# Optimization experiments

Measured on AMD Instinct MI355X. Metric: run time of the kernel, lower is better.

Reference implementation:

```python
import jax, jax.numpy as jnp
import numpy as np
from jax import lax

HID = 512
NEG = -1e30

def conv2d(x, w, pad):
    # x: [N,C,H,W], w: [O,I,kh,kw]
    return lax.conv_general_dilated(x, w, (1, 1), [(pad, pad), (pad, pad)],
                                    dimension_numbers=('NCHW', 'OIHW', 'NCHW'))

def maxpool3s2p1(x):
    return lax.reduce_window(x, -jnp.inf, lax.max, (1, 1, 3, 3), (1, 1, 2, 2),
                             [(0, 0), (0, 0), (1, 1), (1, 1)])

def setup_inputs() -> dict:
    key = jax.random.key(0)
    ks = jax.random.split(key, 12)
    N, B = 128, 16
    gid = jnp.repeat(jnp.arange(B), N // B).astype(jnp.float32)  # sorted group ids
    rois = jnp.concatenate([gid[:, None], jax.random.uniform(ks[0], (N, 4))], axis=1)
    interact_feat = jax.random.normal(ks[1], (N, 2304, 1, 16, 16), jnp.float32)
    bbox_feat = jax.random.normal(ks[2], (N, 1024, 4, 7, 7), jnp.float32)
    s = lambda k, sh: jax.random.normal(k, sh, jnp.float32) * 0.02
    return {
        'rois': rois,
        'interact_feat': interact_feat,
        'bbox_feat': bbox_feat,
        'w_reduce': s(ks[3], (HID, 2304, 1, 1)),
        'w_rsize': s(ks[4], (HID, HID, 3, 3)),
        'wq': s(ks[5], (HID, HID, 3, 3)),
        'wk': s(ks[6], (HID, HID, 3, 3)),
        'wv': s(ks[7], (HID, HID, 3, 3)),
        'w1': s(ks[8], (HID, HID, 3, 3)),
        'gamma': jnp.ones((HID,), jnp.float32),
        'beta': jnp.zeros((HID,), jnp.float32),
        'w_fc': s(ks[9], (HID, 2 * HID)),
    }

def reference(rois, interact_feat, bbox_feat, w_reduce, w_rsize, wq, wk, wv, w1, gamma, beta, w_fc):
    f = interact_feat[:, :, 0]                      # squeeze(2): [N,2304,16,16]
    f = jax.nn.relu(conv2d(f, w_reduce, 0))         # [N,512,16,16]
    f = conv2d(f, w_rsize, 0)                       # no padding -> [N,512,14,14]
    f = maxpool3s2p1(f)                             # [N,512,7,7]

    gid = rois[:, 0].astype(jnp.int32)
    mask = gid[:, None] == gid[None, :]             # [N,N] same-group mask (vectorizes ragged loop)

    q = conv2d(f, wq, 1)
    k = conv2d(f, wk, 1)
    v = conv2d(f, wv, 1)
    # per-pixel attention across rois within each group
    att = jnp.einsum('ichw,jchw->ijhw', q, k) / jnp.sqrt(jnp.asarray(HID, f.dtype))
    att = jnp.where(mask[:, :, None, None], att, NEG)
    att = jax.nn.softmax(att, axis=1)               # softmax over key rois (dim=1)
    virt = jnp.einsum('ijhw,jchw->ichw', att, v)    # [N,512,7,7]

    # GroupNorm(1, C): normalize over (C,H,W), per-channel affine
    mu = virt.mean(axis=(1, 2, 3), keepdims=True)
    var = virt.var(axis=(1, 2, 3), keepdims=True)
    virt = (virt - mu) / jnp.sqrt(var + 1e-5)
    virt = virt * gamma[None, :, None, None] + beta[None, :, None, None]
    virt = jax.nn.relu(virt)
    virt = conv2d(virt, w1, 1)                      # dropout = identity in eval

    ho = (f + virt).mean(axis=(2, 3))               # gap1 -> [N,512]
    ob = bbox_feat.mean(axis=(2, 3, 4))             # gap2 -> [N,1024]
    ob = jax.nn.relu(ob @ w_fc.T)                   # fc1 -> [N,512]
    return jnp.concatenate([ho, ob], axis=1)        # [N,1024]
```

## Files before the change

### kernel.cpp

```cpp
#include <hip/hip_runtime.h>
#include <hip/hip_bf16.h>
#include <math.h>

typedef __bf16 bf16;
typedef __bf16 v8bf __attribute__((ext_vector_type(8)));
typedef float f32x4 __attribute__((ext_vector_type(4)));

#define GLDS16(g, l) __builtin_amdgcn_global_load_lds( \
    (const __attribute__((address_space(1))) void*)(g), \
    (__attribute__((address_space(3))) void*)(l), 16, 0, 0)

__device__ __forceinline__ int xcd_swz(int bid, int nwg) {
  int xcd = bid & 7, off = bid >> 3;
  int q = nwg >> 3, r = nwg & 7;
  return (xcd < r ? xcd * (q + 1) : r * (q + 1) + (xcd - r) * q) + off;
}

#define SBZ __builtin_amdgcn_sched_barrier(0)
#define BARR __builtin_amdgcn_s_barrier()

#define RD_B8(SLOTB) do { \
  _Pragma("unroll") for (int _j = 0; _j < 4; ++_j) \
  _Pragma("unroll") for (int _kk = 0; _kk < 2; ++_kk) { \
    int _r = (wn & 1) * 64 + _j * 16 + l15; \
    int _c = (_kk * 64 + kq) ^ ((_r & 7) << 4); \
    bfr[_j][_kk] = *(const v8bf*)((SLOTB) + _r * 128 + _c); } } while (0)

#define RD_A4(SLOTA, CL) do { \
  _Pragma("unroll") for (int _f = 0; _f < 2; ++_f) \
  _Pragma("unroll") for (int _kk = 0; _kk < 2; ++_kk) { \
    int _r = (CL) * 32 + _f * 16 + l15; \
    int _c = (_kk * 64 + kq) ^ ((_r & 7) << 4); \
    af[_f][_kk] = *(const v8bf*)((SLOTA) + _r * 128 + _c); } } while (0)

#define MMA16(CL) do { \
  __builtin_amdgcn_s_setprio(1); \
  _Pragma("unroll") for (int _f = 0; _f < 2; ++_f) \
  _Pragma("unroll") for (int _j = 0; _j < 4; ++_j) \
  _Pragma("unroll") for (int _kk = 0; _kk < 2; ++_kk) \
    acc[(CL)*2 + _f][_j] = __builtin_amdgcn_mfma_f32_16x16x32_bf16( \
        af[_f][_kk], bfr[_j][_kk], acc[(CL)*2 + _f][_j], 0, 0, 0); \
  __builtin_amdgcn_s_setprio(0); } while (0)

#define VM4 asm volatile("s_waitcnt vmcnt(4)" ::: "memory")
#define VM0 asm volatile("s_waitcnt vmcnt(0)" ::: "memory")

#define PH8_ITER(STGA, STGB, NIT)                                        \
  {                                                                      \
    int t1k = 2 * iv + 1, t2k = 2 * iv + 2, t3k = 2 * iv + 3;            \
    bool s2 = (iv + 1 < (NIT));                                          \
    RD_B8(bslot0); RD_A4(aslot0, 0); STGA(0, t1k, 1);                    \
    SBZ; BARR; SBZ; MMA16(0); SBZ; BARR;                                 \
    RD_A4(aslot0, 1); STGA(1, t1k, 1);                                   \
    SBZ; BARR; SBZ; MMA16(1); SBZ; BARR;                                 \
    RD_A4(aslot0, 2); if (s2) STGB(0, t2k, 0);                           \
    SBZ; BARR; SBZ; MMA16(2); SBZ; BARR;                                 \
    RD_A4(aslot0, 3); if (s2) STGB(1, t2k, 0);                           \
    SBZ; BARR; SBZ; MMA16(3); SBZ;                                       \
    if (s2) { VM4; } else { VM0; }                                       \
    BARR;                                                                \
    RD_B8(bslot1); RD_A4(aslot1, 0); if (s2) STGA(0, t2k, 0);            \
    SBZ; BARR; SBZ; MMA16(0); SBZ; BARR;                                 \
    RD_A4(aslot1, 1); if (s2) STGA(1, t2k, 0);                           \
    SBZ; BARR; SBZ; MMA16(1); SBZ; BARR;                                 \
    RD_A4(aslot1, 2); if (s2) STGB(0, t3k, 1);                           \
    SBZ; BARR; SBZ; MMA16(2); SBZ; BARR;                                 \
    RD_A4(aslot1, 3); if (s2) STGB(1, t3k, 1);                           \
    SBZ; BARR; SBZ; MMA16(3); SBZ;                                       \
    if (s2) { VM4; } else { VM0; }                                       \
    BARR;                                                                \
  }

__global__ __launch_bounds__(512, 2)
void k_gemm_reduce(const bf16* __restrict__ A, const bf16* __restrict__ B,
                   bf16* __restrict__ f1, int mbase)
{
  extern __shared__ char lds[];
  const int s = xcd_swz(blockIdx.x, gridDim.x);
  const int by = s & 1, bx = s >> 1;
  const int t = threadIdx.x, lane = t & 63, w = t >> 6;
  const int wm = w >> 2, wn = w & 3;
  const int l15 = lane & 15, kq = (lane >> 4) << 4;
  const int tr64 = t >> 3;
  const int lb = ((t & 7) << 4) ^ ((tr64 & 7) << 4);
  const int t16 = t * 16;
  const char* aslot0 = lds + wm * 16384;
  const char* aslot1 = lds + 65536 + wm * 16384;
  const char* bslot0 = lds + 32768 + (wn >> 1) * 16384;
  const char* bslot1 = lds + 98304 + (wn >> 1) * 16384;
  const char* paA[2][2]; const char* paB[2][2];
  #pragma unroll
  for (int h = 0; h < 2; ++h)
    #pragma unroll
    for (int c = 0; c < 2; ++c) {
      paA[h][c] = (const char*)A + (size_t)(bx * 256 + h * 128 + c * 64 + tr64) * 4608 + lb;
      paB[h][c] = (const char*)B + (size_t)(by * 256 + h * 128 + c * 64 + tr64) * 4608 + lb;
    }
  #define GR_STGA(h, kt, d) do { \
    GLDS16(paA[h][0] + (size_t)(kt) * 128, lds + (d) * 65536 + (h) * 16384 + t16); \
    GLDS16(paA[h][1] + (size_t)(kt) * 128, lds + (d) * 65536 + (h) * 16384 + 8192 + t16); } while (0)
  #define GR_STGB(h, kt, d) do { \
    GLDS16(paB[h][0] + (size_t)(kt) * 128, lds + (d) * 65536 + 32768 + (h) * 16384 + t16); \
    GLDS16(paB[h][1] + (size_t)(kt) * 128, lds + (d) * 65536 + 32768 + (h) * 16384 + 8192 + t16); } while (0)

  f32x4 acc[8][4] = {};
  v8bf bfr[4][2], af[2][2];
  GR_STGB(0, 0, 0); GR_STGB(1, 0, 0); GR_STGA(0, 0, 0); GR_STGA(1, 0, 0);
  GR_STGB(0, 1, 1); GR_STGB(1, 1, 1);
  VM4; BARR;
  for (int iv = 0; iv < 18; ++iv) PH8_ITER(GR_STGA, GR_STGB, 18);
  const int rbase = (lane >> 4) << 2, cl = lane & 15;
  #pragma unroll
  for (int i = 0; i < 8; ++i)
    #pragma unroll
    for (int j = 0; j < 4; ++j)
      #pragma unroll
      for (int r = 0; r < 4; ++r) {
        int row = mbase + bx * 256 + wm * 128 + i * 16 + rbase + r;
        int col = by * 256 + wn * 64 + j * 16 + cl;
        f1[(size_t)row * 512 + col] = (bf16)fmaxf(acc[i][j][r], 0.f);
      }
}

__global__ __launch_bounds__(512, 2)
void k_conv_rsize(const bf16* __restrict__ f1, const bf16* __restrict__ wt,
                  bf16* __restrict__ f14)
{
  extern __shared__ char lds[];
  const int s = xcd_swz(blockIdx.x, gridDim.x);
  const int by = s & 1, bx = s >> 1;
  const int t = threadIdx.x, lane = t & 63, w = t >> 6;
  const int wm = w >> 2, wn = w & 3;
  const int l15 = lane & 15, kq = (lane >> 4) << 4;
  const int tr64 = t >> 3;
  const int lb = ((t & 7) << 4) ^ ((tr64 & 7) << 4);
  const int t16 = t * 16;
  const char* aslot0 = lds + wm * 16384;
  const char* aslot1 = lds + 65536 + wm * 16384;
  const char* bslot0 = lds + 32768 + (wn >> 1) * 16384;
  const char* bslot1 = lds + 98304 + (wn >> 1) * 16384;
  int ab[2][2]; const char* pwB[2][2];
  #pragma unroll
  for (int h = 0; h < 2; ++h)
    #pragma unroll
    for (int c = 0; c < 2; ++c) {
      int m = bx * 256 + h * 128 + c * 64 + tr64;
      int n = m / 196, rem = m - n * 196;
      int y = rem / 14, x = rem - 14 * (rem / 14);
      ab[h][c] = n * 256 + y * 16 + x;
      pwB[h][c] = (const char*)wt + (size_t)(by * 256 + h * 128 + c * 64 + tr64) * 1024 + lb;
    }
  const char* f1c = (const char*)f1 + lb;
  #define CR_STGA(h, kt, d) do { \
    int _tap = (kt) >> 3, _ko = ((kt) & 7) << 7; \
    int _dy = (_tap * 11) >> 5, _dx = _tap - _dy * 3; \
    int _df = (_dy * 16 + _dx) << 10; \
    GLDS16(f1c + ((size_t)ab[h][0] << 10) + _df + _ko, lds + (d) * 65536 + (h) * 16384 + t16); \
    GLDS16(f1c + ((size_t)ab[h][1] << 10) + _df + _ko, lds + (d) * 65536 + (h) * 16384 + 8192 + t16); } while (0)
  #define CR_STGB(h, kt, d) do { \
    int _tap = (kt) >> 3, _ko = ((kt) & 7) << 7; \
    GLDS16(pwB[h][0] + (size_t)_tap * 524288 + _ko, lds + (d) * 65536 + 32768 + (h) * 16384 + t16); \
    GLDS16(pwB[h][1] + (size_t)_tap * 524288 + _ko, lds + (d) * 65536 + 32768 + (h) * 16384 + 8192 + t16); } while (0)

  f32x4 acc[8][4] = {};
  v8bf bfr[4][2], af[2][2];
  CR_STGB(0, 0, 0); CR_STGB(1, 0, 0); CR_STGA(0, 0, 0); CR_STGA(1, 0, 0);
  CR_STGB(0, 1, 1); CR_STGB(1, 1, 1);
  VM4; BARR;
  for (int iv = 0; iv < 36; ++iv) PH8_ITER(CR_STGA, CR_STGB, 36);
  const int rbase = (lane >> 4) << 2, cl = lane & 15;
  #pragma unroll
  for (int i = 0; i < 8; ++i)
    #pragma unroll
    for (int j = 0; j < 4; ++j)
      #pragma unroll
      for (int r = 0; r < 4; ++r) {
        int row = bx * 256 + wm * 128 + i * 16 + rbase + r;
        int col = by * 256 + wn * 64 + j * 16 + cl;
        f14[(size_t)row * 512 + col] = (bf16)acc[i][j][r];
      }
}

__global__ __launch_bounds__(512, 2)
void k_conv_qkv(const bf16* __restrict__ fin, const bf16* __restrict__ wt,
                bf16* __restrict__ qkv, const bf16* __restrict__ zp,
                const float* __restrict__ bbox, float* __restrict__ obm)
{
  extern __shared__ char lds[];
  const int t = threadIdx.x;
  if (blockIdx.x >= 150) {
    int bid = blockIdx.x - 150;
    int n = bid >> 3;
    int c = (bid & 7) * 128 + (t >> 2);
    int seg = t & 3;
    const float4* p4 = (const float4*)(bbox + ((size_t)n * 1024 + c) * 196);
    float sum = 0.f;
    for (int k = seg; k < 49; k += 4) { float4 ww = p4[k]; sum += ww.x + ww.y + ww.z + ww.w; }
    sum += __shfl_xor(sum, 1);
    sum += __shfl_xor(sum, 2);
    if (seg == 0) obm[n * 1024 + c] = sum * (1.f / 196.f);
    return;
  }
  const int s = xcd_swz(blockIdx.x, 150);
  const int q6 = s % 6, bx = s / 6;
  const int tensor = q6 >> 1, byh = q6 & 1;
  const char* wtc = (const char*)wt + (size_t)tensor * 4718592;
  bf16* outp = qkv + (size_t)tensor * 3211264;
  const int lane = t & 63, w = t >> 6;
  const int wm = w >> 2, wn = w & 3;
  const int l15 = lane & 15, kq = (lane >> 4) << 4;
  const int tr64 = t >> 3;
  const int lb = ((t & 7) << 4) ^ ((tr64 & 7) << 4);
  const int t16 = t * 16;
  const char* aslot0 = lds + wm * 16384;
  const char* aslot1 = lds + 65536 + wm * 16384;
  const char* bslot0 = lds + 32768 + (wn >> 1) * 16384;
  const char* bslot1 = lds + 98304 + (wn >> 1) * 16384;
  int nb[2][2], py[2][2], px[2][2]; const char* pwB[2][2];
  #pragma unroll
  for (int h = 0; h < 2; ++h)
    #pragma unroll
    for (int c = 0; c < 2; ++c) {
      int m = bx * 256 + h * 128 + c * 64 + tr64;
      if (m > 6271) m = 6271;
      int n = m / 49, rem = m - n * 49;
      nb[h][c] = n * 49;
      py[h][c] = rem / 7 - 1;
      px[h][c] = rem - 7 * (rem / 7) - 1;
      pwB[h][c] = wtc + (size_t)(byh * 256 + h * 128 + c * 64 + tr64) * 1024 + lb;
    }
  const char* finc = (const char*)fin + lb;
  const char* zpc = (const char*)zp;
  #define QK_STGA(h, kt, d) do { \
    int _tap = (kt) >> 3, _ko = ((kt) & 7) << 7; \
    int _dy = (_tap * 11) >> 5, _dx = _tap - _dy * 3; \
    _Pragma("unroll") for (int _c = 0; _c < 2; ++_c) { \
      int _iy = py[h][_c] + _dy, _ix = px[h][_c] + _dx; \
      const char* _sp = ((unsigned)_iy < 7u && (unsigned)_ix < 7u) \
          ? finc + (size_t)(nb[h][_c] + _iy * 7 + _ix) * 1024 + _ko : zpc; \
      GLDS16(_sp, lds + (d) * 65536 + (h) * 16384 + _c * 8192 + t16); } } while (0)
  #define QK_STGB(h, kt, d) do { \
    int _tap = (kt) >> 3, _ko = ((kt) & 7) << 7; \
    GLDS16(pwB[h][0] + (size_t)_tap * 524288 + _ko, lds + (d) * 65536 + 32768 + (h) * 16384 + t16); \
    GLDS16(pwB[h][1] + (size_t)_tap * 524288 + _ko, lds + (d) * 65536 + 32768 + (h) * 16384 + 8192 + t16); } while (0)

  f32x4 acc[8][4] = {};
  v8bf bfr[4][2], af[2][2];
  QK_STGB(0, 0, 0); QK_STGB(1, 0, 0); QK_STGA(0, 0, 0); QK_STGA(1, 0, 0);
  QK_STGB(0, 1, 1); QK_STGB(1, 1, 1);
  VM4; BARR;
  for (int iv = 0; iv < 36; ++iv) PH8_ITER(QK_STGA, QK_STGB, 36);
  const int rbase = (lane >> 4) << 2, cl = lane & 15;
  #pragma unroll
  for (int i = 0; i < 8; ++i)
    #pragma unroll
    for (int j = 0; j < 4; ++j)
      #pragma unroll
      for (int r = 0; r < 4; ++r) {
        int row = bx * 256 + wm * 128 + i * 16 + rbase + r;
        if (row < 6272) {
          int col = byh * 256 + wn * 64 + j * 16 + cl;
          outp[(size_t)row * 512 + col] = (bf16)acc[i][j][r];
        }
      }
}

__device__ __forceinline__ void tile_compute(const char* ldsA, const char* ldsB,
                                             f32x4 (&acc)[4][4], int wr, int wc, int lane) {
  const int l15 = lane & 15;
  const int colb = (lane >> 4) << 4;
  #pragma unroll
  for (int kk = 0; kk < 2; ++kk) {
    v8bf a[4], b[4];
    #pragma unroll
    for (int i = 0; i < 4; ++i) {
      int ra = wr * 64 + i * 16 + l15;
      int ca = ((kk << 6) | colb) ^ ((ra & 7) << 4);
      a[i] = *(const v8bf*)(ldsA + ra * 128 + ca);
    }
    #pragma unroll
    for (int j = 0; j < 4; ++j) {
      int rb = wc * 64 + j * 16 + l15;
      int cb = ((kk << 6) | colb) ^ ((rb & 7) << 4);
      b[j] = *(const v8bf*)(ldsB + rb * 128 + cb);
    }
    __builtin_amdgcn_s_setprio(1);
    #pragma unroll
    for (int i = 0; i < 4; ++i)
      #pragma unroll
      for (int j = 0; j < 4; ++j)
        acc[i][j] = __builtin_amdgcn_mfma_f32_16x16x32_bf16(a[i], b[j], acc[i][j], 0, 0, 0);
    __builtin_amdgcn_s_setprio(0);
  }
}

#define PIPELINE_LOOP(NK)                                                   \
  stage(0, lds);                                                            \
  stage(1, lds + 32768);                                                    \
  int cur = 0;                                                              \
  for (int ks = 0; ks < (NK) - 1; ++ks) {                                   \
    asm volatile("s_waitcnt vmcnt(8)" ::: "memory");                        \
    __builtin_amdgcn_s_barrier();                                           \
    __builtin_amdgcn_sched_barrier(0);                                      \
    tile_compute(lds + cur * 32768, lds + cur * 32768 + 16384, acc, wr, wc, lane); \
    __builtin_amdgcn_sched_barrier(0);                                      \
    __builtin_amdgcn_s_barrier();                                           \
    __builtin_amdgcn_sched_barrier(0);                                      \
    if (ks + 2 < (NK)) stage(ks + 2, lds + cur * 32768);                    \
    cur ^= 1;                                                               \
  }                                                                         \
  asm volatile("s_waitcnt vmcnt(0)" ::: "memory");                          \
  __builtin_amdgcn_s_barrier();                                             \
  __builtin_amdgcn_sched_barrier(0);                                        \
  tile_compute(lds + cur * 32768, lds + cur * 32768 + 16384, acc, wr, wc, lane);

__global__ __launch_bounds__(256)
void k_gemm_s(const bf16* __restrict__ A_s, const bf16* __restrict__ w1r,
              float* __restrict__ out)
{
  __shared__ __attribute__((aligned(16))) char lds[65536];
  const int by = blockIdx.x, kspl = blockIdx.y;
  const int t = threadIdx.x, lane = t & 63, w = t >> 6, wr = w >> 1, wc = w & 1;
  const int tr = t >> 3;
  const int cphys = ((t & 7) << 4) ^ ((tr & 7) << 4);
  const char* pa[4]; const char* pb[4];
  #pragma unroll
  for (int i = 0; i < 4; ++i) {
    int r = i * 32 + tr;
    pa[i] = (const char*)A_s + (size_t)r * 9216 + kspl * 2304 + cphys;
    pb[i] = (const char*)w1r + (size_t)(by * 128 + r) * 9216 + kspl * 2304 + cphys;
  }
  const int lo = t * 16;
  auto stage = [&](int ks, char* base) {
    #pragma unroll
    for (int i = 0; i < 4; ++i) GLDS16(pa[i] + ks * 128, base + lo + i * 4096);
    #pragma unroll
    for (int i = 0; i < 4; ++i) GLDS16(pb[i] + ks * 128, base + 16384 + lo + i * 4096);
  };
  f32x4 acc[4][4] = {};
  PIPELINE_LOOP(18)
  const int rb = (lane >> 4) << 2, cl = lane & 15;
  #pragma unroll
  for (int i = 0; i < 4; ++i)
    #pragma unroll
    for (int j = 0; j < 4; ++j)
      #pragma unroll
      for (int r = 0; r < 4; ++r) {
        int row = wr * 64 + i * 16 + rb + r;
        int col = by * 128 + wc * 64 + j * 16 + cl;
        atomicAdd(&out[(size_t)row * 1024 + col], acc[i][j][r]);
      }
}

__global__ void k_tin(const float* __restrict__ in, bf16* __restrict__ A1, int n0)
{
  __shared__ float tile[64][36];
  const int k0 = blockIdx.x * 64, p0 = blockIdx.y * 32, nl = blockIdx.z;
  const int n = n0 + nl;
  const int t = threadIdx.x;
  const float* src = in + (size_t)n * 2304 * 256;
  #pragma unroll
  for (int rep = 0; rep < 2; ++rep) {
    int idx = t + rep * 256;
    int row = idx >> 3, c4 = (idx & 7) * 4;
    float4 v = *(const float4*)(src + (size_t)(k0 + row) * 256 + p0 + c4);
    tile[row][c4] = v.x; tile[row][c4 + 1] = v.y;
    tile[row][c4 + 2] = v.z; tile[row][c4 + 3] = v.w;
  }
  __syncthreads();
  const int pl = t >> 3, ke = (t & 7) * 8;
  v8bf o;
  #pragma unroll
  for (int e = 0; e < 8; ++e) o[e] = (bf16)tile[ke + e][pl];
  bf16* dst = A1 + (size_t)nl * 256 * 2304;
  *(v8bf*)(dst + (size_t)(p0 + pl) * 2304 + k0 + ke) = o;
}

__global__ void k_wprep(const float* __restrict__ wred, const float* __restrict__ s0,
                        const float* __restrict__ s1, const float* __restrict__ s2,
                        const float* __restrict__ s3, const float* __restrict__ s4,
                        bf16* __restrict__ wrb, bf16* __restrict__ wt,
                        bf16* __restrict__ w1r)
{
  if (blockIdx.x < 1152) {
    int idx = (blockIdx.x * 256 + threadIdx.x) * 4;
    float4 v = *(const float4*)(wred + idx);
    bf16* d = wrb + idx;
    d[0] = (bf16)v.x; d[1] = (bf16)v.y; d[2] = (bf16)v.z; d[3] = (bf16)v.w;
    return;
  }
  int bid = blockIdx.x - 1152;
  int by = bid >> 10, bx = bid & 1023;
  const float* src;
  switch (by) {
    case 0: src = s0; break; case 1: src = s1; break; case 2: src = s2; break;
    case 3: src = s3; break; default: src = s4; break;
  }
  int q = bx * 256 + threadIdx.x;
  const float* sp = src + (size_t)q * 9;
  float tmp[9];
  #pragma unroll
  for (int e = 0; e < 9; ++e) tmp[e] = sp[e];
  if (by < 4) {
    bf16* dst = wt + (size_t)by * 2359296;
    #pragma unroll
    for (int e = 0; e < 9; ++e) dst[(size_t)e * 262144 + q] = (bf16)tmp[e];
  } else {
    int co = q >> 9, ci = q & 511;
    #pragma unroll
    for (int e = 0; e < 9; ++e) w1r[(size_t)(co * 9 + e) * 512 + ci] = (bf16)tmp[e];
  }
}

__global__ void k_pool(const bf16* __restrict__ f14, bf16* __restrict__ f7b)
{
  int idx = blockIdx.x * 256 + threadIdx.x;
  int c2 = idx & 255;
  int pp = idx >> 8;
  int n = pp / 49, p7 = pp - n * 49;
  int y = p7 / 7, x = p7 - 7 * (p7 / 7);
  int y0 = 2 * y - 1, x0 = 2 * x - 1;
  const unsigned* f14u = (const unsigned*)f14;
  float m0 = -3.4e38f, m1 = -3.4e38f;
  #pragma unroll
  for (int dy = 0; dy < 3; ++dy) {
    int iy = y0 + dy; if ((unsigned)iy >= 14u) continue;
    #pragma unroll
    for (int dx = 0; dx < 3; ++dx) {
      int ix = x0 + dx; if ((unsigned)ix >= 14u) continue;
      unsigned vv = f14u[(size_t)(n * 196 + iy * 14 + ix) * 256 + c2];
      m0 = fmaxf(m0, __builtin_bit_cast(float, vv << 16));
      m1 = fmaxf(m1, __builtin_bit_cast(float, vv & 0xffff0000u));
    }
  }
  bf16 b0 = (bf16)m0, b1 = (bf16)m1;
  unsigned pk = (unsigned)__builtin_bit_cast(unsigned short, b0)
              | ((unsigned)__builtin_bit_cast(unsigned short, b1) << 16);
  ((unsigned*)f7b)[idx] = pk;
}

__global__ __launch_bounds__(256)
void k_attn(const bf16* __restrict__ q, const bf16* __restrict__ k,
            const bf16* __restrict__ v, const float* __restrict__ rois,
            float* __restrict__ virt)
{
  const int p = blockIdx.x, g = blockIdx.y, t = threadIdx.x;
  __shared__ float sS[8][9];
  __shared__ float sP[8][9];
  __shared__ __attribute__((aligned(16))) bf16 sV[8][512];
  {
    int u = t;
    #pragma unroll
    for (int rep = 0; rep < 2; ++rep, u += 256) {
      int j = u >> 6, ch = u & 63;
      *(v8bf*)&sV[j][ch * 8] = *(const v8bf*)(v + ((size_t)(g * 8 + j) * 49 + p) * 512 + ch * 8);
    }
  }
  int pi = t >> 2, ls = t & 3;
  int i = pi >> 3, j = pi & 7;
  const bf16* qi = q + ((size_t)(g * 8 + i) * 49 + p) * 512;
  const bf16* kj = k + ((size_t)(g * 8 + j) * 49 + p) * 512;
  float s = 0.f;
  for (int ch = ls * 16; ch < ls * 16 + 16; ++ch) {
    v8bf a = *(const v8bf*)(qi + ch * 8);
    v8bf b = *(const v8bf*)(kj + ch * 8);
    #pragma unroll
    for (int e = 0; e < 8; ++e) s += (float)a[e] * (float)b[e];
  }
  s += __shfl_xor(s, 1);
  s += __shfl_xor(s, 2);
  if (ls == 0) sS[i][j] = s * 0.04419417382415922f;
  __syncthreads();
  if (t < 8) {
    float gi = rois[(g * 8 + t) * 5];
    float pv[8]; float mx = -3.4e38f;
    #pragma unroll
    for (int jj = 0; jj < 8; ++jj) {
      float gj = rois[(g * 8 + jj) * 5];
      float sv = (gi == gj) ? sS[t][jj] : -1e30f;
      pv[jj] = sv; mx = fmaxf(mx, sv);
    }
    float sum = 0.f;
    #pragma unroll
    for (int jj = 0; jj < 8; ++jj) { float e = expf(pv[jj] - mx); pv[jj] = e; sum += e; }
    float inv = 1.f / sum;
    #pragma unroll
    for (int jj = 0; jj < 8; ++jj) sP[t][jj] = pv[jj] * inv;
  }
  __syncthreads();
  int i2 = t >> 5, c0 = (t & 31) * 16;
  float o[16];
  #pragma unroll
  for (int e = 0; e < 16; ++e) o[e] = 0.f;
  #pragma unroll
  for (int jj = 0; jj < 8; ++jj) {
    float ww = sP[i2][jj];
    v8bf v0 = *(const v8bf*)&sV[jj][c0];
    v8bf v1 = *(const v8bf*)&sV[jj][c0 + 8];
    #pragma unroll
    for (int e = 0; e < 8; ++e) { o[e] += ww * (float)v0[e]; o[8 + e] += ww * (float)v1[e]; }
  }
  float* dst = virt + ((size_t)(g * 8 + i2) * 49 + p) * 512 + c0;
  #pragma unroll
  for (int e = 0; e < 16; ++e) dst[e] = o[e];
}

__global__ __launch_bounds__(512)
void k_ln_fc(const float* __restrict__ virt, const float* __restrict__ gamma,
             const float* __restrict__ beta, const bf16* __restrict__ f7b,
             bf16* __restrict__ A_s,
             const float* __restrict__ obm, const float* __restrict__ wfc,
             float* __restrict__ out)
{
  const int t = threadIdx.x;
  if (blockIdx.x >= 128) {
    __shared__ float sO[1024];
    int n = blockIdx.x - 128;
    for (int u = t; u < 1024; u += 512) sO[u] = obm[n * 1024 + u];
    __syncthreads();
    const float4* wp = (const float4*)(wfc + (size_t)t * 1024);
    float s = 0.f;
    for (int c4 = 0; c4 < 256; ++c4) {
      float4 w = wp[c4];
      s += w.x * sO[c4 * 4] + w.y * sO[c4 * 4 + 1] + w.z * sO[c4 * 4 + 2] + w.w * sO[c4 * 4 + 3];
    }
    out[n * 1024 + 512 + t] = fmaxf(s, 0.f);
    return;
  }
  const int n = blockIdx.x;
  const float* p = virt + (size_t)n * 25088 + t;
  float xv[49];
  float s1 = 0.f, s2 = 0.f;
  #pragma unroll
  for (int pp = 0; pp < 49; ++pp) {
    float x = p[pp * 512];
    xv[pp] = x; s1 += x; s2 += x * x;
  }
  __shared__ float r1[512], r2[512];
  r1[t] = s1; r2[t] = s2; __syncthreads();
  for (int off = 256; off; off >>= 1) {
    if (t < off) { r1[t] += r1[t + off]; r2[t] += r2[t + off]; }
    __syncthreads();
  }
  float mu = r1[0] * (1.f / 25088.f);
  float var = r2[0] * (1.f / 25088.f) - mu * mu;
  float rstd = rsqrtf(var + 1e-5f);
  float g = gamma[t], be = beta[t];
  const bf16* fp = f7b + (size_t)n * 25088 + t;
  float T = 0, R0 = 0, R6 = 0, C0 = 0, C6 = 0;
  float X00 = 0, X06 = 0, X60 = 0, X66 = 0, F = 0;
  #pragma unroll
  for (int pp = 0; pp < 49; ++pp) {
    const int u = pp / 7, v = pp - 7 * (pp / 7);
    float y = fmaxf((xv[pp] - mu) * rstd * g + be, 0.f);
    T += y;
    if (u == 0) R0 += y;
    if (u == 6) R6 += y;
    if (v == 0) C0 += y;
    if (v == 6) C6 += y;
    if (pp == 0)  X00 = y;
    if (pp == 6)  X06 = y;
    if (pp == 42) X60 = y;
    if (pp == 48) X66 = y;
    F += (float)fp[pp * 512];
  }
  float sv[9] = { T-R6-C6+X66, T-R6, T-R6-C0+X60,
                  T-C6,        T,    T-C0,
                  T-R0-C6+X06, T-R0, T-R0-C0+X00 };
  bf16* Ap = A_s + (size_t)n * 4608 + t;
  #pragma unroll
  for (int tap = 0; tap < 9; ++tap)
    Ap[tap * 512] = (bf16)(sv[tap] * (1.f / 49.f));
  out[n * 1024 + t] = F * (1.f / 49.f);
}

extern "C" void kernel_launch(void* const* d_in, const int* in_sizes, int n_in,
                              void* d_out, int out_size, void* d_ws, size_t ws_size,
                              hipStream_t stream) {
  const float* rois     = (const float*)d_in[0];
  const float* interact = (const float*)d_in[1];
  const float* bbox     = (const float*)d_in[2];
  const float* w_reduce = (const float*)d_in[3];
  const float* w_rsize  = (const float*)d_in[4];
  const float* wq       = (const float*)d_in[5];
  const float* wk       = (const float*)d_in[6];
  const float* wv       = (const float*)d_in[7];
  const float* w1       = (const float*)d_in[8];
  const float* gamma    = (const float*)d_in[9];
  const float* beta     = (const float*)d_in[10];
  const float* wfc      = (const float*)d_in[11];
  float* out = (float*)d_out;
  char* ws = (char*)d_ws;

  size_t o = 0;
  auto take = [&](size_t sz) { size_t r = o; o += (sz + 255) & ~(size_t)255; return r; };
  bf16*  wrb   = (bf16*)(ws + take(2359296));
  bf16*  wt    = (bf16*)(ws + take(18874368));
  bf16*  w1r   = (bf16*)(ws + take(4718592));
  char*  Rf1   = ws + take(33554432);
  bf16*  f7b   = (bf16*)(ws + take(6422528));
  float* virt  = (float*)(ws + take(12845056));
  bf16*  A_s   = (bf16*)(ws + take(1179648));
  float* obm   = (float*)(ws + take(524288));
  bf16*  zp    = (bf16*)(ws + take(256));
  size_t fixedEnd = o;
  const size_t A1_FULL = 150994944;
  bool full = (ws_size >= fixedEnd + A1_FULL);
  bf16* A1  = (bf16*)(ws + fixedEnd);
  bf16* f14 = (bf16*)(ws + fixedEnd);

  bf16* f1 = (bf16*)Rf1;
  bf16* qb = (bf16*)Rf1;
  bf16* kb = qb + 3211264;
  bf16* vb = kb + 3211264;

  hipMemsetAsync(zp, 0, 256, stream);

  k_wprep<<<6272, 256, 0, stream>>>(w_reduce, w_rsize, wq, wk, wv, w1, wrb, wt, w1r);

  if (full) {
    k_tin<<<dim3(36, 8, 128), 256, 0, stream>>>(interact, A1, 0);
    k_gemm_reduce<<<256, 512, 131072, stream>>>(A1, wrb, f1, 0);
  } else {
    for (int ch = 0; ch < 4; ++ch) {
      k_tin<<<dim3(36, 8, 32), 256, 0, stream>>>(interact, A1, ch * 32);
      k_gemm_reduce<<<64, 512, 131072, stream>>>(A1, wrb, f1, ch * 8192);
    }
  }

  k_conv_rsize<<<196, 512, 131072, stream>>>(f1, wt, f14);
  k_pool<<<6272, 256, 0, stream>>>(f14, f7b);

  k_conv_qkv<<<1174, 512, 131072, stream>>>(f7b, wt + (size_t)1 * 2359296, qb, zp, bbox, obm);

  k_attn<<<dim3(49, 16), 256, 0, stream>>>(qb, kb, vb, rois, virt);

  k_ln_fc<<<256, 512, 0, stream>>>(virt, gamma, beta, f7b, A_s, obm, wfc, out);

  k_gemm_s<<<dim3(4, 4), 256, 0, stream>>>(A_s, w1r, out);
}
```

Measured before the change: 514.7 us.

## Overlap input transpose of next chunk with reduce GEMM of current chunk

Fuses the weight-prep kernel with the first chunk's input transpose into one launch. The 1x1 reduce GEMM is then split into four chunked launches, and each launch also carries the blocks that transpose the next chunk's input. The aim is to hide the memory-bound transpose behind the compute-bound GEMM and cut kernel launches. The cost is heavy extra blocks that each reserve 128KB of dynamic LDS, so transpose blocks may limit occupancy. The full-workspace path is dropped, so the GEMM always runs as four 64-block launches.

```diff
diff --git a/kernel.cpp b/kernel.cpp
--- a/kernel.cpp
+++ b/kernel.cpp
@@ -71,14 +71,93 @@
     BARR;                                                                \
   }
 
+__device__ __forceinline__ void tin_block(const float* __restrict__ in,
+                                          bf16* __restrict__ A1,
+                                          int n, int kt, int pt, int t, char* ldsbuf)
+{
+  float* tile = (float*)ldsbuf;
+  const int k0 = kt * 64, p0 = pt * 64;
+  const float* src = in + (size_t)n * 589824;
+  #pragma unroll
+  for (int rep = 0; rep < 2; ++rep) {
+    int idx = t + rep * 512;
+    int row = idx >> 4, c4 = (idx & 15) * 4;
+    float4 v = *(const float4*)(src + (size_t)(k0 + row) * 256 + p0 + c4);
+    tile[row * 69 + c4]     = v.x; tile[row * 69 + c4 + 1] = v.y;
+    tile[row * 69 + c4 + 2] = v.z; tile[row * 69 + c4 + 3] = v.w;
+  }
+  __syncthreads();
+  const int pl = t >> 3, ke = (t & 7) * 8;
+  v8bf o;
+  #pragma unroll
+  for (int e = 0; e < 8; ++e) o[e] = (bf16)tile[(ke + e) * 69 + pl];
+  *(v8bf*)(A1 + (size_t)(n * 256 + p0 + pl) * 2304 + k0 + ke) = o;
+}
+
+__global__ __launch_bounds__(512)
+void k_prep(const float* __restrict__ interact, bf16* __restrict__ A1,
+            const float* __restrict__ wred, const float* __restrict__ s0,
+            const float* __restrict__ s1, const float* __restrict__ s2,
+            const float* __restrict__ s3, const float* __restrict__ s4,
+            bf16* __restrict__ wrb, bf16* __restrict__ wt,
+            bf16* __restrict__ w1r)
+{
+  __shared__ __attribute__((aligned(16))) char ldsb[17664];
+  const int t = threadIdx.x;
+  if (blockIdx.x < 4608) {
+    int bid = blockIdx.x;
+    int kt = bid % 36, rest = bid / 36;
+    int pt = rest & 3, nl = rest >> 2;
+    tin_block(interact, A1, nl, kt, pt, t, ldsb);
+    return;
+  }
+  int bid2 = blockIdx.x - 4608;
+  if (bid2 < 576) {
+    int idx = (bid2 * 512 + t) * 4;
+    float4 v = *(const float4*)(wred + idx);
+    bf16* d = wrb + idx;
+    d[0] = (bf16)v.x; d[1] = (bf16)v.y; d[2] = (bf16)v.z; d[3] = (bf16)v.w;
+    return;
+  }
+  int bid3 = bid2 - 576;
+  int by = bid3 >> 9, bx = bid3 & 511;
+  const float* src;
+  switch (by) {
+    case 0: src = s0; break; case 1: src = s1; break; case 2: src = s2; break;
+    case 3: src = s3; break; default: src = s4; break;
+  }
+  int q = bx * 512 + t;
+  const float* sp = src + (size_t)q * 9;
+  float tmp[9];
+  #pragma unroll
+  for (int e = 0; e < 9; ++e) tmp[e] = sp[e];
+  if (by < 4) {
+    bf16* dst = wt + (size_t)by * 2359296;
+    #pragma unroll
+    for (int e = 0; e < 9; ++e) dst[(size_t)e * 262144 + q] = (bf16)tmp[e];
+  } else {
+    int co = q >> 9, ci = q & 511;
+    #pragma unroll
+    for (int e = 0; e < 9; ++e) w1r[(size_t)(co * 9 + e) * 512 + ci] = (bf16)tmp[e];
+  }
+}
+
 __global__ __launch_bounds__(512, 2)
-void k_gemm_reduce(const bf16* __restrict__ A, const bf16* __restrict__ B,
-                   bf16* __restrict__ f1, int mbase)
+void k_tg(const float* __restrict__ interact, bf16* __restrict__ A1,
+          const bf16* __restrict__ B, bf16* __restrict__ f1, int chunk)
 {
   extern __shared__ char lds[];
-  const int s = xcd_swz(blockIdx.x, gridDim.x);
-  const int by = s & 1, bx = s >> 1;
-  const int t = threadIdx.x, lane = t & 63, w = t >> 6;
+  const int t = threadIdx.x;
+  if (blockIdx.x >= 64) {
+    int bid = blockIdx.x - 64;
+    int kt = bid % 36, rest = bid / 36;
+    int pt = rest & 3, nl = rest >> 2;
+    tin_block(interact, A1, (chunk + 1) * 32 + nl, kt, pt, t, lds);
+    return;
+  }
+  const int s = xcd_swz(blockIdx.x, 64);
+  const int by = s & 1, bx = chunk * 32 + (s >> 1);
+  const int lane = t & 63, w = t >> 6;
   const int wm = w >> 2, wn = w & 3;
   const int l15 = lane & 15, kq = (lane >> 4) << 4;
   const int tr64 = t >> 3;
@@ -93,22 +172,22 @@
   for (int h = 0; h < 2; ++h)
     #pragma unroll
     for (int c = 0; c < 2; ++c) {
-      paA[h][c] = (const char*)A + (size_t)(bx * 256 + h * 128 + c * 64 + tr64) * 4608 + lb;
+      paA[h][c] = (const char*)A1 + (size_t)(bx * 256 + h * 128 + c * 64 + tr64) * 4608 + lb;
       paB[h][c] = (const char*)B + (size_t)(by * 256 + h * 128 + c * 64 + tr64) * 4608 + lb;
     }
-  #define GR_STGA(h, kt, d) do { \
+  #define GT_STGA(h, kt, d) do { \
     GLDS16(paA[h][0] + (size_t)(kt) * 128, lds + (d) * 65536 + (h) * 16384 + t16); \
     GLDS16(paA[h][1] + (size_t)(kt) * 128, lds + (d) * 65536 + (h) * 16384 + 8192 + t16); } while (0)
-  #define GR_STGB(h, kt, d) do { \
+  #define GT_STGB(h, kt, d) do { \
     GLDS16(paB[h][0] + (size_t)(kt) * 128, lds + (d) * 65536 + 32768 + (h) * 16384 + t16); \
     GLDS16(paB[h][1] + (size_t)(kt) * 128, lds + (d) * 65536 + 32768 + (h) * 16384 + 8192 + t16); } while (0)
 
   f32x4 acc[8][4] = {};
   v8bf bfr[4][2], af[2][2];
-  GR_STGB(0, 0, 0); GR_STGB(1, 0, 0); GR_STGA(0, 0, 0); GR_STGA(1, 0, 0);
-  GR_STGB(0, 1, 1); GR_STGB(1, 1, 1);
+  GT_STGB(0, 0, 0); GT_STGB(1, 0, 0); GT_STGA(0, 0, 0); GT_STGA(1, 0, 0);
+  GT_STGB(0, 1, 1); GT_STGB(1, 1, 1);
   VM4; BARR;
-  for (int iv = 0; iv < 18; ++iv) PH8_ITER(GR_STGA, GR_STGB, 18);
+  for (int iv = 0; iv < 18; ++iv) PH8_ITER(GT_STGA, GT_STGB, 18);
   const int rbase = (lane >> 4) << 2, cl = lane & 15;
   #pragma unroll
   for (int i = 0; i < 8; ++i)
@@ -116,7 +195,7 @@
     for (int j = 0; j < 4; ++j)
       #pragma unroll
       for (int r = 0; r < 4; ++r) {
-        int row = mbase + bx * 256 + wm * 128 + i * 16 + rbase + r;
+        int row = bx * 256 + wm * 128 + i * 16 + rbase + r;
         int col = by * 256 + wn * 64 + j * 16 + cl;
         f1[(size_t)row * 512 + col] = (bf16)fmaxf(acc[i][j][r], 0.f);
       }
@@ -352,66 +431,6 @@
       }
 }
 
-__global__ void k_tin(const float* __restrict__ in, bf16* __restrict__ A1, int n0)
-{
-  __shared__ float tile[64][36];
-  const int k0 = blockIdx.x * 64, p0 = blockIdx.y * 32, nl = blockIdx.z;
-  const int n = n0 + nl;
-  const int t = threadIdx.x;
-  const float* src = in + (size_t)n * 2304 * 256;
-  #pragma unroll
-  for (int rep = 0; rep < 2; ++rep) {
-    int idx = t + rep * 256;
-    int row = idx >> 3, c4 = (idx & 7) * 4;
-    float4 v = *(const float4*)(src + (size_t)(k0 + row) * 256 + p0 + c4);
-    tile[row][c4] = v.x; tile[row][c4 + 1] = v.y;
-    tile[row][c4 + 2] = v.z; tile[row][c4 + 3] = v.w;
-  }
-  __syncthreads();
-  const int pl = t >> 3, ke = (t & 7) * 8;
-  v8bf o;
-  #pragma unroll
-  for (int e = 0; e < 8; ++e) o[e] = (bf16)tile[ke + e][pl];
-  bf16* dst = A1 + (size_t)nl * 256 * 2304;
-  *(v8bf*)(dst + (size_t)(p0 + pl) * 2304 + k0 + ke) = o;
-}
-
-__global__ void k_wprep(const float* __restrict__ wred, const float* __restrict__ s0,
-                        const float* __restrict__ s1, const float* __restrict__ s2,
-                        const float* __restrict__ s3, const float* __restrict__ s4,
-                        bf16* __restrict__ wrb, bf16* __restrict__ wt,
-                        bf16* __restrict__ w1r)
-{
-  if (blockIdx.x < 1152) {
-    int idx = (blockIdx.x * 256 + threadIdx.x) * 4;
-    float4 v = *(const float4*)(wred + idx);
-    bf16* d = wrb + idx;
-    d[0] = (bf16)v.x; d[1] = (bf16)v.y; d[2] = (bf16)v.z; d[3] = (bf16)v.w;
-    return;
-  }
-  int bid = blockIdx.x - 1152;
-  int by = bid >> 10, bx = bid & 1023;
-  const float* src;
-  switch (by) {
-    case 0: src = s0; break; case 1: src = s1; break; case 2: src = s2; break;
-    case 3: src = s3; break; default: src = s4; break;
-  }
-  int q = bx * 256 + threadIdx.x;
-  const float* sp = src + (size_t)q * 9;
-  float tmp[9];
-  #pragma unroll
-  for (int e = 0; e < 9; ++e) tmp[e] = sp[e];
-  if (by < 4) {
-    bf16* dst = wt + (size_t)by * 2359296;
-    #pragma unroll
-    for (int e = 0; e < 9; ++e) dst[(size_t)e * 262144 + q] = (bf16)tmp[e];
-  } else {
-    int co = q >> 9, ci = q & 511;
-    #pragma unroll
-    for (int e = 0; e < 9; ++e) w1r[(size_t)(co * 9 + e) * 512 + ci] = (bf16)tmp[e];
-  }
-}
-
 __global__ void k_pool(const bf16* __restrict__ f14, bf16* __restrict__ f7b)
 {
   int idx = blockIdx.x * 256 + threadIdx.x;
@@ -604,8 +623,6 @@
   float* obm   = (float*)(ws + take(524288));
   bf16*  zp    = (bf16*)(ws + take(256));
   size_t fixedEnd = o;
-  const size_t A1_FULL = 150994944;
-  bool full = (ws_size >= fixedEnd + A1_FULL);
   bf16* A1  = (bf16*)(ws + fixedEnd);
   bf16* f14 = (bf16*)(ws + fixedEnd);
 
@@ -616,17 +633,12 @@
 
   hipMemsetAsync(zp, 0, 256, stream);
 
-  k_wprep<<<6272, 256, 0, stream>>>(w_reduce, w_rsize, wq, wk, wv, w1, wrb, wt, w1r);
-
-  if (full) {
-    k_tin<<<dim3(36, 8, 128), 256, 0, stream>>>(interact, A1, 0);
-    k_gemm_reduce<<<256, 512, 131072, stream>>>(A1, wrb, f1, 0);
-  } else {
-    for (int ch = 0; ch < 4; ++ch) {
-      k_tin<<<dim3(36, 8, 32), 256, 0, stream>>>(interact, A1, ch * 32);
-      k_gemm_reduce<<<64, 512, 131072, stream>>>(A1, wrb, f1, ch * 8192);
-    }
-  }
+  k_prep<<<7744, 512, 0, stream>>>(interact, A1, w_reduce, w_rsize, wq, wk, wv, w1,
+                                   wrb, wt, w1r);
+  k_tg<<<4672, 512, 131072, stream>>>(interact, A1, wrb, f1, 0);
+  k_tg<<<4672, 512, 131072, stream>>>(interact, A1, wrb, f1, 1);
+  k_tg<<<4672, 512, 131072, stream>>>(interact, A1, wrb, f1, 2);
+  k_tg<<<64, 512, 131072, stream>>>(interact, A1, wrb, f1, 3);
 
   k_conv_rsize<<<196, 512, 131072, stream>>>(f1, wt, f14);
   k_pool<<<6272, 256, 0, stream>>>(f14, f7b);
```

Measured after the change: 598.6 us. +16.3%, slower.
